# Kernel tuning notes

Measured on AMD Instinct MI355X. Metric: run time of the kernel, lower is better.

## Reference

```python
import jax, jax.numpy as jnp
import numpy as np

BATCH = 131072
FEAS = 256
K = 256
DEPTH = 3


def setup_inputs() -> dict:
    key = jax.random.key(0)
    ks = jax.random.split(key, 16)
    # deep tower dims: k//1 -> k//2 -> k//3 -> k//4  == 256 -> 128 -> 85 -> 64
    dims = [K // i for i in range(1, DEPTH + 2)]
    inp = {
        "x": jax.random.normal(ks[0], (BATCH, FEAS), jnp.float32),
        "w_wide": jax.random.normal(ks[1], (FEAS, 1), jnp.float32) * 0.02,
        "b_wide": jnp.zeros((1,), jnp.float32),
        # nn.Parameter(torch.rand(feas, k)) -> uniform [0,1)
        "V": jax.random.uniform(ks[2], (FEAS, K), jnp.float32),
    }
    for i in range(DEPTH):
        fan_in, fan_out = dims[i], dims[i + 1]
        inp[f"w{i+1}"] = jax.random.normal(ks[3 + 2 * i], (fan_in, fan_out), jnp.float32) * (1.0 / np.sqrt(fan_in))
        inp[f"b{i+1}"] = jnp.zeros((fan_out,), jnp.float32)
    inp["w_out"] = jax.random.normal(ks[12], (dims[-1], 1), jnp.float32) * (1.0 / np.sqrt(dims[-1]))
    inp["b_out"] = jnp.zeros((1,), jnp.float32)
    return inp


def reference(x, w_wide, b_wide, V, w1, b1, w2, b2, w3, b3, w_out, b_out):
    # wide (linear) part: [B, 1]
    linear = x @ w_wide + b_wide
    # FM bi-interaction pooling. Original loop: sum_{j >= i} x_i x_j (v_i * v_j)
    # (break/continue on zeros only skip zero-valued terms). Including the
    # diagonal, this equals 0.5 * ((x @ V)^2 + (x^2) @ (V^2)).  [B, K]
    xv = x @ V
    x2v2 = (x * x) @ (V * V)
    tmp = 0.5 * (xv * xv + x2v2)
    # deep tower: Linear + ReLU at each depth
    for w, b in ((w1, b1), (w2, b2), (w3, b3)):
        tmp = jax.nn.relu(tmp @ w + b)
    deep_out = tmp @ w_out + b_out  # [B, 1]
    return jax.nn.sigmoid(linear + deep_out)
```

## Files before the change

kernel.cpp:

```cpp
#include <hip/hip_runtime.h>
#include <math.h>


typedef _Float16 f16;
typedef _Float16 f16x8 __attribute__((ext_vector_type(8)));
typedef float f32x4 __attribute__((ext_vector_type(4)));

#define NROWS   131072
#define ROWS    64
#define FDIM    256
#define KDIM    256
#define D1      128
#define D2      85
#define D2P     96

#define FSW(mm) ((((mm) & 7)) ^ ((((mm) >> 3) & 1) << 1))

#define OFF_VT_H   0x0UL
#define OFF_VT_L   0x20000UL
#define OFF_V2T    0x40000UL
#define OFF_W1T_H  0x60000UL
#define OFF_W1T_L  0x70000UL
#define OFF_W2T_H  0x80000UL
#define OFF_W2T_L  0x86000UL
#define OFF_W3T_H  0x8C000UL
#define OFF_W3T_L  0x8F000UL

static __device__ __forceinline__ f32x4 mfma16(f16x8 a, f16x8 b, f32x4 c) {
  return __builtin_amdgcn_mfma_f32_16x16x32_f16(a, b, c, 0, 0, 0);
}

static __device__ __forceinline__ void barrier_lgkm() {
  __builtin_amdgcn_sched_barrier(0);
  asm volatile("s_waitcnt lgkmcnt(0)" ::: "memory");
  __builtin_amdgcn_s_barrier();
  asm volatile("" ::: "memory");
  __builtin_amdgcn_sched_barrier(0);
}

__global__ __launch_bounds__(256) void prep_kernel(
    const float* __restrict__ V, const float* __restrict__ w1,
    const float* __restrict__ w2, const float* __restrict__ w3,
    f16* VT_h, f16* VT_l, f16* V2T,
    f16* W1T_h, f16* W1T_l, f16* W2T_h, f16* W2T_l, f16* W3T_h, f16* W3T_l) {
  int idx0 = blockIdx.x * 256 + threadIdx.x;
  int stride = gridDim.x * 256;
  for (int idx = idx0; idx < KDIM * FDIM; idx += stride) {
    int i = idx >> 8, k = idx & 255;
    float v = V[idx];
    f16 h = (f16)v;
    int o = k * FDIM + i;
    VT_h[o] = h;
    VT_l[o] = (f16)(v - (float)h);
    V2T[o] = (f16)(v * v);
  }
  for (int idx = idx0; idx < D1 * KDIM; idx += stride) {
    int k = idx >> 7, n = idx & 127;
    float w = w1[idx];
    f16 h = (f16)w;
    int o = n * KDIM + k;
    W1T_h[o] = h;
    W1T_l[o] = (f16)(w - (float)h);
  }
  for (int idx = idx0; idx < D2P * D1; idx += stride) {
    int n = idx >> 7, k = idx & 127;
    float w = (n < D2) ? w2[k * D2 + n] : 0.f;
    f16 h = (f16)w;
    W2T_h[idx] = h;
    W2T_l[idx] = (f16)(w - (float)h);
  }
  for (int idx = idx0; idx < 64 * D2P; idx += stride) {
    int n = idx / D2P, k = idx - n * D2P;
    float w = (k < D2) ? w3[k * 64 + n] : 0.f;
    f16 h = (f16)w;
    W3T_h[idx] = h;
    W3T_l[idx] = (f16)(w - (float)h);
  }
}

__global__ __launch_bounds__(512, 4) void fused_kernel(
    const float* __restrict__ x, const float* __restrict__ w_wide,
    const float* __restrict__ b_wide,
    const f16* __restrict__ VT_h, const f16* __restrict__ VT_l,
    const f16* __restrict__ V2T,
    const f16* __restrict__ W1T_h, const f16* __restrict__ W1T_l,
    const float* __restrict__ b1,
    const f16* __restrict__ W2T_h, const f16* __restrict__ W2T_l,
    const float* __restrict__ b2,
    const f16* __restrict__ W3T_h, const f16* __restrict__ W3T_l,
    const float* __restrict__ b3,
    const float* __restrict__ w_out, const float* __restrict__ b_out,
    float* __restrict__ out) {
  __shared__ __align__(16) f16 smem[32768];
  __shared__ float linS[ROWS];
  __shared__ float pfS[ROWS * 2];

  f16* tmpH = smem;
  f16* tmpL = smem + 16384;
  f16* h1H  = smem + 16384;
  f16* h1L  = smem + 24576;
  f16* h2H  = smem;
  f16* h2L  = smem + 8192;

  const int tid = threadIdx.x;
  const int lane = tid & 63, wv = tid >> 6;
  const int q = lane >> 4, ln = lane & 15;
  const int row0 = blockIdx.x * ROWS;
  const int srow = tid >> 3;
  const int u8 = (tid & 7) << 3;
  const int stg = srow * 64 + (((tid & 7) ^ (srow & 7)) << 3);
  const int fr = (ln & 7) ^ (((ln >> 3) & 1) << 1);

  f32x4 accV[4][2], acc2[4][2];
#pragma unroll
  for (int i = 0; i < 4; ++i)
#pragma unroll
    for (int j = 0; j < 2; ++j) {
      accV[i][j] = (f32x4){0.f, 0.f, 0.f, 0.f};
      acc2[i][j] = (f32x4){0.f, 0.f, 0.f, 0.f};
    }
  float linp = 0.f;

  float4 aP[2][2], wP[2][2];

#define LOADG(C, P)                                                         \
  {                                                                         \
    const float* xp = x + (size_t)(row0 + srow) * FDIM + (C) * 64 + u8;     \
    const float* wp = w_wide + (C) * 64 + u8;                               \
    aP[P][0] = *(const float4*)(xp);                                        \
    aP[P][1] = *(const float4*)(xp + 4);                                    \
    wP[P][0] = *(const float4*)(wp);                                        \
    wP[P][1] = *(const float4*)(wp + 4);                                    \
  }

#define STAGE(P)                                                            \
  {                                                                         \
    f16* bb = smem + (P) * 12288;                                           \
    float v[8] = {aP[P][0].x, aP[P][0].y, aP[P][0].z, aP[P][0].w,           \
                  aP[P][1].x, aP[P][1].y, aP[P][1].z, aP[P][1].w};          \
    float w[8] = {wP[P][0].x, wP[P][0].y, wP[P][0].z, wP[P][0].w,           \
                  wP[P][1].x, wP[P][1].y, wP[P][1].z, wP[P][1].w};          \
    f16x8 hh, ll, ss;                                                       \
    _Pragma("unroll") for (int j = 0; j < 8; ++j) {                         \
      linp += v[j] * w[j];                                                  \
      f16 h = (f16)v[j];                                                    \
      hh[j] = h;                                                            \
      ll[j] = (f16)(v[j] - (float)h);                                       \
      ss[j] = (f16)(v[j] * v[j]);                                           \
    }                                                                       \
    *(f16x8*)(bb + stg) = hh;                                               \
    *(f16x8*)(bb + 4096 + stg) = ll;                                        \
    *(f16x8*)(bb + 8192 + stg) = ss;                                        \
  }

  LOADG(0, 0);
  STAGE(0);
  LOADG(1, 1);
  barrier_lgkm();

#pragma unroll
  for (int c = 0; c < 4; ++c) {
    if (c < 2) LOADG(c + 2, c & 1);
    if (c < 3) STAGE((c + 1) & 1);
    f16* sb = smem + (c & 1) * 12288;
#pragma unroll
    for (int ksl = 0; ksl < 2; ++ksl) {
      const int k0 = c * 64 + ksl * 32;
      f16x8 Bh[2], Bl[2], B2[2];
#pragma unroll
      for (int ni = 0; ni < 2; ++ni) {
        int n = wv * 32 + ni * 16 + ln;
        size_t boff = (size_t)n * FDIM + k0 + q * 8;
        Bh[ni] = *(const f16x8*)(VT_h + boff);
        Bl[ni] = *(const f16x8*)(VT_l + boff);
        B2[ni] = *(const f16x8*)(V2T + boff);
      }
#pragma unroll
      for (int mi = 0; mi < 4; ++mi) {
        int aoff = (mi * 16 + ln) * 64 + ((((ksl << 2) + q) ^ (ln & 7)) << 3);
        f16x8 Ah = *(const f16x8*)(sb + aoff);
        f16x8 Al = *(const f16x8*)(sb + 4096 + aoff);
        f16x8 A2 = *(const f16x8*)(sb + 8192 + aoff);
#pragma unroll
        for (int ni = 0; ni < 2; ++ni) {
          accV[mi][ni] = mfma16(Al, Bh[ni], accV[mi][ni]);
          accV[mi][ni] = mfma16(Ah, Bl[ni], accV[mi][ni]);
          accV[mi][ni] = mfma16(Ah, Bh[ni], accV[mi][ni]);
          acc2[mi][ni] = mfma16(A2, B2[ni], acc2[mi][ni]);
        }
      }
    }
    barrier_lgkm();
  }
#undef LOADG
#undef STAGE

  {
    float s0 = linp;
    s0 += __shfl_xor(s0, 1);
    s0 += __shfl_xor(s0, 2);
    s0 += __shfl_xor(s0, 4);
    if ((tid & 7) == 0) linS[srow] = s0 + b_wide[0];
  }

#pragma unroll
  for (int mi = 0; mi < 4; ++mi)
#pragma unroll
    for (int r = 0; r < 4; ++r) {
      int m = mi * 16 + q * 4 + r;
      int mrow = m * 256, fw = FSW(q * 4 + r);
#pragma unroll
      for (int ni = 0; ni < 2; ++ni) {
        int n = wv * 32 + ni * 16 + ln;
        float xv = accV[mi][ni][r];
        float val = 0.5f * (xv * xv + acc2[mi][ni][r]);
        f16 hi = (f16)val;
        f16 lo = (f16)(val - (float)hi);
        int off = mrow + (((n >> 3) ^ fw) << 3) + (n & 7);
        tmpH[off] = hi;
        tmpL[off] = lo;
      }
    }

  barrier_lgkm();

  f32x4 acc1[4];
#pragma unroll
  for (int i = 0; i < 4; ++i) acc1[i] = (f32x4){0.f, 0.f, 0.f, 0.f};

#pragma unroll
  for (int ks = 0; ks < 8; ++ks) {
    size_t boff = (size_t)(wv * 16 + ln) * KDIM + ks * 32 + q * 8;
    f16x8 Bh = *(const f16x8*)(W1T_h + boff);
    f16x8 Bl = *(const f16x8*)(W1T_l + boff);
#pragma unroll
    for (int mi = 0; mi < 4; ++mi) {
      int m = mi * 16 + ln;
      int aoff = m * 256 + (((ks * 4 + q) ^ fr) << 3);
      f16x8 Ah = *(const f16x8*)(tmpH + aoff);
      f16x8 Al = *(const f16x8*)(tmpL + aoff);
      acc1[mi] = mfma16(Al, Bh, acc1[mi]);
      acc1[mi] = mfma16(Ah, Bl, acc1[mi]);
      acc1[mi] = mfma16(Ah, Bh, acc1[mi]);
    }
  }

  barrier_lgkm();

  {
    int n = wv * 16 + ln;
    float bias = b1[n];
#pragma unroll
    for (int mi = 0; mi < 4; ++mi)
#pragma unroll
      for (int r = 0; r < 4; ++r) {
        int m = mi * 16 + q * 4 + r;
        float z = acc1[mi][r] + bias;
        z = z > 0.f ? z : 0.f;
        f16 hi = (f16)z;
        f16 lo = (f16)(z - (float)hi);
        int off = m * 128 + (((n >> 3) ^ FSW(q * 4 + r)) << 3) + (n & 7);
        h1H[off] = hi;
        h1L[off] = lo;
      }
  }

  barrier_lgkm();

  const int mt = wv & 3, half = wv >> 2;
  f32x4 accL2[3];
#pragma unroll
  for (int j = 0; j < 3; ++j) accL2[j] = (f32x4){0.f, 0.f, 0.f, 0.f};

#pragma unroll
  for (int ks = 0; ks < 4; ++ks) {
    int m = mt * 16 + ln;
    int aoff = m * 128 + (((ks * 4 + q) ^ fr) << 3);
    f16x8 Ah = *(const f16x8*)(h1H + aoff);
    f16x8 Al = *(const f16x8*)(h1L + aoff);
#pragma unroll
    for (int nj = 0; nj < 3; ++nj) {
      int n = (half * 3 + nj) * 16 + ln;
      size_t boff = (size_t)n * D1 + ks * 32 + q * 8;
      f16x8 Bh = *(const f16x8*)(W2T_h + boff);
      f16x8 Bl = *(const f16x8*)(W2T_l + boff);
      accL2[nj] = mfma16(Al, Bh, accL2[nj]);
      accL2[nj] = mfma16(Ah, Bl, accL2[nj]);
      accL2[nj] = mfma16(Ah, Bh, accL2[nj]);
    }
  }

#pragma unroll
  for (int r = 0; r < 4; ++r) {
    int m = mt * 16 + q * 4 + r;
    int mrow = m * 128, fw = FSW(q * 4 + r);
#pragma unroll
    for (int nj = 0; nj < 3; ++nj) {
      int n = (half * 3 + nj) * 16 + ln;
      float z = accL2[nj][r] + ((n < D2) ? b2[n] : 0.f);
      z = z > 0.f ? z : 0.f;
      f16 hi = (f16)z;
      f16 lo = (f16)(z - (float)hi);
      int off = mrow + (((n >> 3) ^ fw) << 3) + (n & 7);
      h2H[off] = hi;
      h2L[off] = lo;
    }
  }

  barrier_lgkm();

  f32x4 accL3[2];
  accL3[0] = (f32x4){0.f, 0.f, 0.f, 0.f};
  accL3[1] = (f32x4){0.f, 0.f, 0.f, 0.f};

#pragma unroll
  for (int ks = 0; ks < 3; ++ks) {
    int m = mt * 16 + ln;
    int aoff = m * 128 + (((ks * 4 + q) ^ fr) << 3);
    f16x8 Ah = *(const f16x8*)(h2H + aoff);
    f16x8 Al = *(const f16x8*)(h2L + aoff);
#pragma unroll
    for (int nj = 0; nj < 2; ++nj) {
      int n = (half * 2 + nj) * 16 + ln;
      size_t boff = (size_t)n * D2P + ks * 32 + q * 8;
      f16x8 Bh = *(const f16x8*)(W3T_h + boff);
      f16x8 Bl = *(const f16x8*)(W3T_l + boff);
      accL3[nj] = mfma16(Al, Bh, accL3[nj]);
      accL3[nj] = mfma16(Ah, Bl, accL3[nj]);
      accL3[nj] = mfma16(Ah, Bh, accL3[nj]);
    }
  }

  {
    float b3v[2], wov[2];
#pragma unroll
    for (int nj = 0; nj < 2; ++nj) {
      int n = (half * 2 + nj) * 16 + ln;
      b3v[nj] = b3[n];
      wov[nj] = w_out[n];
    }
#pragma unroll
    for (int r = 0; r < 4; ++r) {
      float part = 0.f;
#pragma unroll
      for (int nj = 0; nj < 2; ++nj) {
        float z = accL3[nj][r] + b3v[nj];
        part += (z > 0.f ? z : 0.f) * wov[nj];
      }
      part += __shfl_xor(part, 1);
      part += __shfl_xor(part, 2);
      part += __shfl_xor(part, 4);
      part += __shfl_xor(part, 8);
      if (ln == 0) pfS[(mt * 16 + q * 4 + r) * 2 + half] = part;
    }
  }

  __syncthreads();

  if (tid < ROWS) {
    float zf = linS[tid] + pfS[tid * 2] + pfS[tid * 2 + 1] + b_out[0];
    out[row0 + tid] = 1.f / (1.f + expf(-zf));
  }
}

extern "C" void kernel_launch(void* const* d_in, const int* in_sizes, int n_in,
                              void* d_out, int out_size, void* d_ws, size_t ws_size,
                              hipStream_t stream) {
  const float* x = (const float*)d_in[0];
  const float* w_wide = (const float*)d_in[1];
  const float* b_wide = (const float*)d_in[2];
  const float* V = (const float*)d_in[3];
  const float* w1 = (const float*)d_in[4];
  const float* b1 = (const float*)d_in[5];
  const float* w2 = (const float*)d_in[6];
  const float* b2 = (const float*)d_in[7];
  const float* w3 = (const float*)d_in[8];
  const float* b3 = (const float*)d_in[9];
  const float* w_out = (const float*)d_in[10];
  const float* b_out = (const float*)d_in[11];
  float* out = (float*)d_out;
  char* ws = (char*)d_ws;

  f16* VT_h = (f16*)(ws + OFF_VT_H);
  f16* VT_l = (f16*)(ws + OFF_VT_L);
  f16* V2T = (f16*)(ws + OFF_V2T);
  f16* W1T_h = (f16*)(ws + OFF_W1T_H);
  f16* W1T_l = (f16*)(ws + OFF_W1T_L);
  f16* W2T_h = (f16*)(ws + OFF_W2T_H);
  f16* W2T_l = (f16*)(ws + OFF_W2T_L);
  f16* W3T_h = (f16*)(ws + OFF_W3T_H);
  f16* W3T_l = (f16*)(ws + OFF_W3T_L);

  prep_kernel<<<256, 256, 0, stream>>>(V, w1, w2, w3, VT_h, VT_l, V2T, W1T_h,
                                       W1T_l, W2T_h, W2T_l, W3T_h, W3T_l);

  fused_kernel<<<NROWS / ROWS, 512, 0, stream>>>(
      x, w_wide, b_wide, VT_h, VT_l, V2T, W1T_h, W1T_l, b1, W2T_h, W2T_l, b2,
      W3T_h, W3T_l, b3, w_out, b_out, out);
}
```

Baseline: 376.8 us.

## Make fused kernel persistent and prefetch next tile's input during deep-tower stages

The fused kernel now launches a fixed grid of 512 blocks, and each block loops over four 64-row tiles instead of handling one. While the current tile runs its MLP layers, the first x chunk of the next tile is loaded from global memory and staged into shared memory. This is meant to hide global-load latency behind compute and to cut block launch overhead. Shared-memory buffers for h1 and h2 are swapped so the prefetch staging area does not collide with live data. The cost is fewer resident blocks to hide latency, and a schedule that depends on getting the buffer aliasing exactly right.

Result: slower. 643.0 us (+70.7%).

```diff
diff --git a/kernel.cpp b/kernel.cpp
--- a/kernel.cpp
+++ b/kernel.cpp
@@ -13,6 +13,9 @@
 #define D1      128
 #define D2      85
 #define D2P     96
+#define GRID    512
+#define NTILES  (NROWS / ROWS)
+#define TPB     (NTILES / GRID)
 
 #define FSW(mm) ((((mm) & 7)) ^ ((((mm) >> 3) & 1) << 1))
 
@@ -97,35 +100,25 @@
 
   f16* tmpH = smem;
   f16* tmpL = smem + 16384;
-  f16* h1H  = smem + 16384;
-  f16* h1L  = smem + 24576;
-  f16* h2H  = smem;
-  f16* h2L  = smem + 8192;
+  f16* h1H  = smem;
+  f16* h1L  = smem + 8192;
+  f16* h2H  = smem + 16384;
+  f16* h2L  = smem + 24576;
 
   const int tid = threadIdx.x;
   const int lane = tid & 63, wv = tid >> 6;
   const int q = lane >> 4, ln = lane & 15;
-  const int row0 = blockIdx.x * ROWS;
   const int srow = tid >> 3;
   const int u8 = (tid & 7) << 3;
   const int stg = srow * 64 + (((tid & 7) ^ (srow & 7)) << 3);
   const int fr = (ln & 7) ^ (((ln >> 3) & 1) << 1);
-
-  f32x4 accV[4][2], acc2[4][2];
-#pragma unroll
-  for (int i = 0; i < 4; ++i)
-#pragma unroll
-    for (int j = 0; j < 2; ++j) {
-      accV[i][j] = (f32x4){0.f, 0.f, 0.f, 0.f};
-      acc2[i][j] = (f32x4){0.f, 0.f, 0.f, 0.f};
-    }
-  float linp = 0.f;
+  const int mt = wv & 3, half = wv >> 2;
 
   float4 aP[2][2], wP[2][2];
 
-#define LOADG(C, P)                                                         \
+#define LOADG(R0, C, P)                                                     \
   {                                                                         \
-    const float* xp = x + (size_t)(row0 + srow) * FDIM + (C) * 64 + u8;     \
+    const float* xp = x + (size_t)((R0) + srow) * FDIM + (C) * 64 + u8;     \
     const float* wp = w_wide + (C) * 64 + u8;                               \
     aP[P][0] = *(const float4*)(xp);                                        \
     aP[P][1] = *(const float4*)(xp + 4);                                    \
@@ -133,7 +126,7 @@
     wP[P][1] = *(const float4*)(wp + 4);                                    \
   }
 
-#define STAGE(P)                                                            \
+#define STAGE(P, LACC)                                                      \
   {                                                                         \
     f16* bb = smem + (P) * 12288;                                           \
     float v[8] = {aP[P][0].x, aP[P][0].y, aP[P][0].z, aP[P][0].w,           \
@@ -142,7 +135,7 @@
                   wP[P][1].x, wP[P][1].y, wP[P][1].z, wP[P][1].w};          \
     f16x8 hh, ll, ss;                                                       \
     _Pragma("unroll") for (int j = 0; j < 8; ++j) {                         \
-      linp += v[j] * w[j];                                                  \
+      LACC += v[j] * w[j];                                                  \
       f16 h = (f16)v[j];                                                    \
       hh[j] = h;                                                            \
       ll[j] = (f16)(v[j] - (float)h);                                       \
@@ -153,214 +146,244 @@
     *(f16x8*)(bb + 8192 + stg) = ss;                                        \
   }
 
-  LOADG(0, 0);
-  STAGE(0);
-  LOADG(1, 1);
-  barrier_lgkm();
-
-#pragma unroll
-  for (int c = 0; c < 4; ++c) {
-    if (c < 2) LOADG(c + 2, c & 1);
-    if (c < 3) STAGE((c + 1) & 1);
-    f16* sb = smem + (c & 1) * 12288;
-#pragma unroll
-    for (int ksl = 0; ksl < 2; ++ksl) {
-      const int k0 = c * 64 + ksl * 32;
-      f16x8 Bh[2], Bl[2], B2[2];
-#pragma unroll
-      for (int ni = 0; ni < 2; ++ni) {
-        int n = wv * 32 + ni * 16 + ln;
-        size_t boff = (size_t)n * FDIM + k0 + q * 8;
-        Bh[ni] = *(const f16x8*)(VT_h + boff);
-        Bl[ni] = *(const f16x8*)(VT_l + boff);
-        B2[ni] = *(const f16x8*)(V2T + boff);
-      }
-#pragma unroll
-      for (int mi = 0; mi < 4; ++mi) {
-        int aoff = (mi * 16 + ln) * 64 + ((((ksl << 2) + q) ^ (ln & 7)) << 3);
-        f16x8 Ah = *(const f16x8*)(sb + aoff);
-        f16x8 Al = *(const f16x8*)(sb + 4096 + aoff);
-        f16x8 A2 = *(const f16x8*)(sb + 8192 + aoff);
+  float linpN = 0.f;
+
+#pragma unroll 1
+  for (int it = 0; it < TPB; ++it) {
+    const int row0 = (blockIdx.x + it * GRID) * ROWS;
+
+    f32x4 accV[4][2], acc2[4][2];
+#pragma unroll
+    for (int i = 0; i < 4; ++i)
+#pragma unroll
+      for (int j = 0; j < 2; ++j) {
+        accV[i][j] = (f32x4){0.f, 0.f, 0.f, 0.f};
+        acc2[i][j] = (f32x4){0.f, 0.f, 0.f, 0.f};
+      }
+    float linp;
+
+    if (it == 0) {
+      linp = 0.f;
+      LOADG(row0, 0, 0);
+      STAGE(0, linp);
+      LOADG(row0, 1, 1);
+      barrier_lgkm();
+    } else {
+      linp = linpN;
+      LOADG(row0, 1, 1);
+    }
+
+#pragma unroll
+    for (int c = 0; c < 4; ++c) {
+      if (c < 2) LOADG(row0, c + 2, c & 1);
+      if (c < 3) STAGE((c + 1) & 1, linp);
+      f16* sb = smem + (c & 1) * 12288;
+#pragma unroll
+      for (int ksl = 0; ksl < 2; ++ksl) {
+        const int k0 = c * 64 + ksl * 32;
+        f16x8 Bh[2], Bl[2], B2[2];
 #pragma unroll
         for (int ni = 0; ni < 2; ++ni) {
-          accV[mi][ni] = mfma16(Al, Bh[ni], accV[mi][ni]);
-          accV[mi][ni] = mfma16(Ah, Bl[ni], accV[mi][ni]);
-          accV[mi][ni] = mfma16(Ah, Bh[ni], accV[mi][ni]);
-          acc2[mi][ni] = mfma16(A2, B2[ni], acc2[mi][ni]);
+          int n = wv * 32 + ni * 16 + ln;
+          size_t boff = (size_t)n * FDIM + k0 + q * 8;
+          Bh[ni] = *(const f16x8*)(VT_h + boff);
+          Bl[ni] = *(const f16x8*)(VT_l + boff);
+          B2[ni] = *(const f16x8*)(V2T + boff);
         }
-      }
-    }
-    barrier_lgkm();
-  }
-#undef LOADG
-#undef STAGE
-
-  {
-    float s0 = linp;
-    s0 += __shfl_xor(s0, 1);
-    s0 += __shfl_xor(s0, 2);
-    s0 += __shfl_xor(s0, 4);
-    if ((tid & 7) == 0) linS[srow] = s0 + b_wide[0];
-  }
-
-#pragma unroll
-  for (int mi = 0; mi < 4; ++mi)
-#pragma unroll
-    for (int r = 0; r < 4; ++r) {
-      int m = mi * 16 + q * 4 + r;
-      int mrow = m * 256, fw = FSW(q * 4 + r);
-#pragma unroll
-      for (int ni = 0; ni < 2; ++ni) {
-        int n = wv * 32 + ni * 16 + ln;
-        float xv = accV[mi][ni][r];
-        float val = 0.5f * (xv * xv + acc2[mi][ni][r]);
-        f16 hi = (f16)val;
-        f16 lo = (f16)(val - (float)hi);
-        int off = mrow + (((n >> 3) ^ fw) << 3) + (n & 7);
-        tmpH[off] = hi;
-        tmpL[off] = lo;
-      }
-    }
-
-  barrier_lgkm();
-
-  f32x4 acc1[4];
-#pragma unroll
-  for (int i = 0; i < 4; ++i) acc1[i] = (f32x4){0.f, 0.f, 0.f, 0.f};
-
-#pragma unroll
-  for (int ks = 0; ks < 8; ++ks) {
-    size_t boff = (size_t)(wv * 16 + ln) * KDIM + ks * 32 + q * 8;
-    f16x8 Bh = *(const f16x8*)(W1T_h + boff);
-    f16x8 Bl = *(const f16x8*)(W1T_l + boff);
-#pragma unroll
-    for (int mi = 0; mi < 4; ++mi) {
-      int m = mi * 16 + ln;
-      int aoff = m * 256 + (((ks * 4 + q) ^ fr) << 3);
-      f16x8 Ah = *(const f16x8*)(tmpH + aoff);
-      f16x8 Al = *(const f16x8*)(tmpL + aoff);
-      acc1[mi] = mfma16(Al, Bh, acc1[mi]);
-      acc1[mi] = mfma16(Ah, Bl, acc1[mi]);
-      acc1[mi] = mfma16(Ah, Bh, acc1[mi]);
-    }
-  }
-
-  barrier_lgkm();
-
-  {
-    int n = wv * 16 + ln;
-    float bias = b1[n];
+#pragma unroll
+        for (int mi = 0; mi < 4; ++mi) {
+          int aoff =
+              (mi * 16 + ln) * 64 + ((((ksl << 2) + q) ^ (ln & 7)) << 3);
+          f16x8 Ah = *(const f16x8*)(sb + aoff);
+          f16x8 Al = *(const f16x8*)(sb + 4096 + aoff);
+          f16x8 A2 = *(const f16x8*)(sb + 8192 + aoff);
+#pragma unroll
+          for (int ni = 0; ni < 2; ++ni) {
+            accV[mi][ni] = mfma16(Al, Bh[ni], accV[mi][ni]);
+            accV[mi][ni] = mfma16(Ah, Bl[ni], accV[mi][ni]);
+            accV[mi][ni] = mfma16(Ah, Bh[ni], accV[mi][ni]);
+            acc2[mi][ni] = mfma16(A2, B2[ni], acc2[mi][ni]);
+          }
+        }
+      }
+      barrier_lgkm();
+    }
+
+    {
+      float s0 = linp;
+      s0 += __shfl_xor(s0, 1);
+      s0 += __shfl_xor(s0, 2);
+      s0 += __shfl_xor(s0, 4);
+      if ((tid & 7) == 0) linS[srow] = s0 + b_wide[0];
+    }
+
 #pragma unroll
     for (int mi = 0; mi < 4; ++mi)
 #pragma unroll
       for (int r = 0; r < 4; ++r) {
         int m = mi * 16 + q * 4 + r;
-        float z = acc1[mi][r] + bias;
+        int mrow = m * 256, fw = FSW(q * 4 + r);
+#pragma unroll
+        for (int ni = 0; ni < 2; ++ni) {
+          int n = wv * 32 + ni * 16 + ln;
+          float xv = accV[mi][ni][r];
+          float val = 0.5f * (xv * xv + acc2[mi][ni][r]);
+          f16 hi = (f16)val;
+          f16 lo = (f16)(val - (float)hi);
+          int off = mrow + (((n >> 3) ^ fw) << 3) + (n & 7);
+          tmpH[off] = hi;
+          tmpL[off] = lo;
+        }
+      }
+
+    barrier_lgkm();
+
+    f32x4 acc1[4];
+#pragma unroll
+    for (int i = 0; i < 4; ++i) acc1[i] = (f32x4){0.f, 0.f, 0.f, 0.f};
+
+#pragma unroll
+    for (int ks = 0; ks < 8; ++ks) {
+      size_t boff = (size_t)(wv * 16 + ln) * KDIM + ks * 32 + q * 8;
+      f16x8 Bh = *(const f16x8*)(W1T_h + boff);
+      f16x8 Bl = *(const f16x8*)(W1T_l + boff);
+#pragma unroll
+      for (int mi = 0; mi < 4; ++mi) {
+        int m = mi * 16 + ln;
+        int aoff = m * 256 + (((ks * 4 + q) ^ fr) << 3);
+        f16x8 Ah = *(const f16x8*)(tmpH + aoff);
+        f16x8 Al = *(const f16x8*)(tmpL + aoff);
+        acc1[mi] = mfma16(Al, Bh, acc1[mi]);
+        acc1[mi] = mfma16(Ah, Bl, acc1[mi]);
+        acc1[mi] = mfma16(Ah, Bh, acc1[mi]);
+      }
+    }
+
+    barrier_lgkm();
+
+    {
+      int n = wv * 16 + ln;
+      float bias = b1[n];
+#pragma unroll
+      for (int mi = 0; mi < 4; ++mi)
+#pragma unroll
+        for (int r = 0; r < 4; ++r) {
+          int m = mi * 16 + q * 4 + r;
+          float z = acc1[mi][r] + bias;
+          z = z > 0.f ? z : 0.f;
+          f16 hi = (f16)z;
+          f16 lo = (f16)(z - (float)hi);
+          int off = m * 128 + (((n >> 3) ^ FSW(q * 4 + r)) << 3) + (n & 7);
+          h1H[off] = hi;
+          h1L[off] = lo;
+        }
+    }
+
+    barrier_lgkm();
+
+    if (it < TPB - 1) LOADG(row0 + GRID * ROWS, 0, 0);
+
+    f32x4 accL2[3];
+#pragma unroll
+    for (int j = 0; j < 3; ++j) accL2[j] = (f32x4){0.f, 0.f, 0.f, 0.f};
+
+#pragma unroll
+    for (int ks = 0; ks < 4; ++ks) {
+      int m = mt * 16 + ln;
+      int aoff = m * 128 + (((ks * 4 + q) ^ fr) << 3);
+      f16x8 Ah = *(const f16x8*)(h1H + aoff);
+      f16x8 Al = *(const f16x8*)(h1L + aoff);
+#pragma unroll
+      for (int nj = 0; nj < 3; ++nj) {
+        int n = (half * 3 + nj) * 16 + ln;
+        size_t boff = (size_t)n * D1 + ks * 32 + q * 8;
+        f16x8 Bh = *(const f16x8*)(W2T_h + boff);
+        f16x8 Bl = *(const f16x8*)(W2T_l + boff);
+        accL2[nj] = mfma16(Al, Bh, accL2[nj]);
+        accL2[nj] = mfma16(Ah, Bl, accL2[nj]);
+        accL2[nj] = mfma16(Ah, Bh, accL2[nj]);
+      }
+    }
+
+#pragma unroll
+    for (int r = 0; r < 4; ++r) {
+      int m = mt * 16 + q * 4 + r;
+      int mrow = m * 128, fw = FSW(q * 4 + r);
+#pragma unroll
+      for (int nj = 0; nj < 3; ++nj) {
+        int n = (half * 3 + nj) * 16 + ln;
+        float z = accL2[nj][r] + ((n < D2) ? b2[n] : 0.f);
         z = z > 0.f ? z : 0.f;
         f16 hi = (f16)z;
         f16 lo = (f16)(z - (float)hi);
-        int off = m * 128 + (((n >> 3) ^ FSW(q * 4 + r)) << 3) + (n & 7);
-        h1H[off] = hi;
-        h1L[off] = lo;
-      }
-  }
-
-  barrier_lgkm();
-
-  const int mt = wv & 3, half = wv >> 2;
-  f32x4 accL2[3];
-#pragma unroll
-  for (int j = 0; j < 3; ++j) accL2[j] = (f32x4){0.f, 0.f, 0.f, 0.f};
-
-#pragma unroll
-  for (int ks = 0; ks < 4; ++ks) {
-    int m = mt * 16 + ln;
-    int aoff = m * 128 + (((ks * 4 + q) ^ fr) << 3);
-    f16x8 Ah = *(const f16x8*)(h1H + aoff);
-    f16x8 Al = *(const f16x8*)(h1L + aoff);
-#pragma unroll
-    for (int nj = 0; nj < 3; ++nj) {
-      int n = (half * 3 + nj) * 16 + ln;
-      size_t boff = (size_t)n * D1 + ks * 32 + q * 8;
-      f16x8 Bh = *(const f16x8*)(W2T_h + boff);
-      f16x8 Bl = *(const f16x8*)(W2T_l + boff);
-      accL2[nj] = mfma16(Al, Bh, accL2[nj]);
-      accL2[nj] = mfma16(Ah, Bl, accL2[nj]);
-      accL2[nj] = mfma16(Ah, Bh, accL2[nj]);
-    }
-  }
-
-#pragma unroll
-  for (int r = 0; r < 4; ++r) {
-    int m = mt * 16 + q * 4 + r;
-    int mrow = m * 128, fw = FSW(q * 4 + r);
-#pragma unroll
-    for (int nj = 0; nj < 3; ++nj) {
-      int n = (half * 3 + nj) * 16 + ln;
-      float z = accL2[nj][r] + ((n < D2) ? b2[n] : 0.f);
-      z = z > 0.f ? z : 0.f;
-      f16 hi = (f16)z;
-      f16 lo = (f16)(z - (float)hi);
-      int off = mrow + (((n >> 3) ^ fw) << 3) + (n & 7);
-      h2H[off] = hi;
-      h2L[off] = lo;
-    }
-  }
-
-  barrier_lgkm();
-
-  f32x4 accL3[2];
-  accL3[0] = (f32x4){0.f, 0.f, 0.f, 0.f};
-  accL3[1] = (f32x4){0.f, 0.f, 0.f, 0.f};
-
-#pragma unroll
-  for (int ks = 0; ks < 3; ++ks) {
-    int m = mt * 16 + ln;
-    int aoff = m * 128 + (((ks * 4 + q) ^ fr) << 3);
-    f16x8 Ah = *(const f16x8*)(h2H + aoff);
-    f16x8 Al = *(const f16x8*)(h2L + aoff);
-#pragma unroll
-    for (int nj = 0; nj < 2; ++nj) {
-      int n = (half * 2 + nj) * 16 + ln;
-      size_t boff = (size_t)n * D2P + ks * 32 + q * 8;
-      f16x8 Bh = *(const f16x8*)(W3T_h + boff);
-      f16x8 Bl = *(const f16x8*)(W3T_l + boff);
-      accL3[nj] = mfma16(Al, Bh, accL3[nj]);
-      accL3[nj] = mfma16(Ah, Bl, accL3[nj]);
-      accL3[nj] = mfma16(Ah, Bh, accL3[nj]);
-    }
-  }
-
-  {
-    float b3v[2], wov[2];
-#pragma unroll
-    for (int nj = 0; nj < 2; ++nj) {
-      int n = (half * 2 + nj) * 16 + ln;
-      b3v[nj] = b3[n];
-      wov[nj] = w_out[n];
-    }
-#pragma unroll
-    for (int r = 0; r < 4; ++r) {
-      float part = 0.f;
+        int off = mrow + (((n >> 3) ^ fw) << 3) + (n & 7);
+        h2H[off] = hi;
+        h2L[off] = lo;
+      }
+    }
+
+    barrier_lgkm();
+
+    if (it < TPB - 1) {
+      linpN = 0.f;
+      STAGE(0, linpN);
+    }
+
+    f32x4 accL3[2];
+    accL3[0] = (f32x4){0.f, 0.f, 0.f, 0.f};
+    accL3[1] = (f32x4){0.f, 0.f, 0.f, 0.f};
+
+#pragma unroll
+    for (int ks = 0; ks < 3; ++ks) {
+      int m = mt * 16 + ln;
+      int aoff = m * 128 + (((ks * 4 + q) ^ fr) << 3);
+      f16x8 Ah = *(const f16x8*)(h2H + aoff);
+      f16x8 Al = *(const f16x8*)(h2L + aoff);
 #pragma unroll
       for (int nj = 0; nj < 2; ++nj) {
-        float z = accL3[nj][r] + b3v[nj];
-        part += (z > 0.f ? z : 0.f) * wov[nj];
-      }
-      part += __shfl_xor(part, 1);
-      part += __shfl_xor(part, 2);
-      part += __shfl_xor(part, 4);
-      part += __shfl_xor(part, 8);
-      if (ln == 0) pfS[(mt * 16 + q * 4 + r) * 2 + half] = part;
-    }
-  }
-
-  __syncthreads();
-
-  if (tid < ROWS) {
-    float zf = linS[tid] + pfS[tid * 2] + pfS[tid * 2 + 1] + b_out[0];
-    out[row0 + tid] = 1.f / (1.f + expf(-zf));
-  }
+        int n = (half * 2 + nj) * 16 + ln;
+        size_t boff = (size_t)n * D2P + ks * 32 + q * 8;
+        f16x8 Bh = *(const f16x8*)(W3T_h + boff);
+        f16x8 Bl = *(const f16x8*)(W3T_l + boff);
+        accL3[nj] = mfma16(Al, Bh, accL3[nj]);
+        accL3[nj] = mfma16(Ah, Bl, accL3[nj]);
+        accL3[nj] = mfma16(Ah, Bh, accL3[nj]);
+      }
+    }
+
+    {
+      float b3v[2], wov[2];
+#pragma unroll
+      for (int nj = 0; nj < 2; ++nj) {
+        int n = (half * 2 + nj) * 16 + ln;
+        b3v[nj] = b3[n];
+        wov[nj] = w_out[n];
+      }
+#pragma unroll
+      for (int r = 0; r < 4; ++r) {
+        float part = 0.f;
+#pragma unroll
+        for (int nj = 0; nj < 2; ++nj) {
+          float z = accL3[nj][r] + b3v[nj];
+          part += (z > 0.f ? z : 0.f) * wov[nj];
+        }
+        part += __shfl_xor(part, 1);
+        part += __shfl_xor(part, 2);
+        part += __shfl_xor(part, 4);
+        part += __shfl_xor(part, 8);
+        if (ln == 0) pfS[(mt * 16 + q * 4 + r) * 2 + half] = part;
+      }
+    }
+
+    barrier_lgkm();
+
+    if (tid < ROWS) {
+      float zf = linS[tid] + pfS[tid * 2] + pfS[tid * 2 + 1] + b_out[0];
+      out[row0 + tid] = 1.f / (1.f + expf(-zf));
+    }
+  }
+#undef LOADG
+#undef STAGE
 }
 
 extern "C" void kernel_launch(void* const* d_in, const int* in_sizes, int n_in,
@@ -394,7 +417,7 @@
   prep_kernel<<<256, 256, 0, stream>>>(V, w1, w2, w3, VT_h, VT_l, V2T, W1T_h,
                                        W1T_l, W2T_h, W2T_l, W3T_h, W3T_l);
 
-  fused_kernel<<<NROWS / ROWS, 512, 0, stream>>>(
+  fused_kernel<<<GRID, 512, 0, stream>>>(
       x, w_wide, b_wide, VT_h, VT_l, V2T, W1T_h, W1T_l, b1, W2T_h, W2T_l, b2,
       W3T_h, W3T_l, b3, w_out, b_out, out);
 }
```
